# Performance work log

Hardware: AMD Instinct MI355X
Metric: run time of the kernel (lower is better)

Reference implementation:

```python
import jax, jax.numpy as jnp
import numpy as np

DILATIONS = (1, 3, 5)
NUM_HEADS = 2


def _conv(x, w, b, dil=1, pad=0):
    # x: [B,C,H,W], w: [O,I,kh,kw] (OIHW), 'same'-style padding = dilation for k=3
    y = jax.lax.conv_general_dilated(
        x, w, window_strides=(1, 1), padding=[(pad, pad), (pad, pad)],
        rhs_dilation=(dil, dil), dimension_numbers=('NCHW', 'OIHW', 'NCHW'))
    return y + b[None, :, None, None]


def setup_inputs() -> dict:
    key = jax.random.key(0)
    ks = jax.random.split(key, 4)
    B, Cin, H, W = 4, 256, 64, 64
    Cout = 256
    x = jax.random.normal(ks[0], (B, Cin, H, W), dtype=jnp.float32)
    # kaiming-uniform-like init scale
    q_w = jax.random.uniform(ks[1], (Cout, Cin, 3, 3), dtype=jnp.float32,
                             minval=-1.0, maxval=1.0) * np.sqrt(6.0 / (Cin * 9))
    k_w = jax.random.uniform(ks[2], (Cout, Cin, 1, 1), dtype=jnp.float32,
                             minval=-1.0, maxval=1.0) * np.sqrt(6.0 / Cin)
    v_w = jax.random.uniform(ks[3], (Cout, Cin, 1, 1), dtype=jnp.float32,
                             minval=-1.0, maxval=1.0) * np.sqrt(6.0 / Cin)
    q_b = jnp.zeros((Cout,), jnp.float32)
    k_b = jnp.zeros((Cout,), jnp.float32)
    v_b = jnp.zeros((Cout,), jnp.float32)
    return {"x": x, "q_w": q_w, "q_b": q_b, "k_w": k_w, "k_b": k_b,
            "v_w": v_w, "v_b": v_b}


def reference(x, q_w, q_b, k_w, k_b, v_w, v_b):
    B, C, H, W = x.shape
    Cout = q_w.shape[0]
    hd = Cout // NUM_HEADS  # head_dim
    # ds_conv2d: sum of SiLU(dilated conv) over dilations 1,3,5 (padding=dilation)
    q = sum(jax.nn.silu(_conv(x, q_w, q_b, dil=d, pad=d)) for d in DILATIONS)
    k = _conv(x, k_w, k_b)
    v = _conv(x, v_w, v_b)
    N = H * W
    # [B, heads, head_dim, N]
    q = q.reshape(B, NUM_HEADS, hd, N)
    k = k.reshape(B, NUM_HEADS, hd, N)
    v = v.reshape(B, NUM_HEADS, hd, N)
    # energy[b,h,n,m] = sum_d q[b,h,d,n] * k[b,h,d,m]
    energy = jnp.einsum('bhdn,bhdm->bhnm', q, k)
    attn = jax.nn.softmax(energy / jnp.sqrt(jnp.float32(hd)), axis=-1)
    # out[b,h,n,d] = sum_m attn[b,h,n,m] * v[b,h,d,m]; then back to [B,C,H,W]
    out = jnp.einsum('bhnm,bhdm->bhdn', attn, v)
    return out.reshape(B, Cout, H, W)
```

## Files before the change

### kernel.cpp

```cpp
#include <hip/hip_runtime.h>
#include <cstdint>

typedef __attribute__((ext_vector_type(8))) _Float16 f16x8;
typedef __attribute__((ext_vector_type(4))) float f32x4;

#define DEV static __device__ __forceinline__

DEV void gld_lds16(void* lds_base, const void* gsrc) {
  __builtin_amdgcn_global_load_lds(
      (const __attribute__((address_space(1))) unsigned int*)gsrc,
      (__attribute__((address_space(3))) unsigned int*)lds_base,
      16, 0, 0);
}
DEV unsigned short f2h(float f) {
  _Float16 h = (_Float16)f;
  return __builtin_bit_cast(unsigned short, h);
}
DEV unsigned pk2h(float a, float b) {
  auto h2 = __builtin_amdgcn_cvt_pkrtz(a, b);
  return __builtin_bit_cast(unsigned, h2);
}
DEV float v_exp2(float x) { float r; asm("v_exp_f32 %0, %1" : "=v"(r) : "v"(x)); return r; }
DEV float v_rcp(float x) { float r; asm("v_rcp_f32 %0, %1" : "=v"(r) : "v"(x)); return r; }


__global__ __launch_bounds__(256) void k_prep_x(
    const float* __restrict__ x, char* __restrict__ xpad,
    const float* __restrict__ qw, const float* __restrict__ kw, const float* __restrict__ vw,
    unsigned short* __restrict__ Wq, unsigned short* __restrict__ Wk, unsigned short* __restrict__ Wv) {
  __shared__ float xs[32 * 257];
  int h = blockIdx.x, b = blockIdx.y, t = threadIdx.x;
  int gid = (b * 64 + h) * 256 + t;
  const float* q9 = qw + (size_t)gid * 9;
#pragma unroll
  for (int tp = 0; tp < 9; tp++) Wq[tp * 65536 + gid] = f2h(q9[tp]);
  Wk[gid] = f2h(kw[gid]);
  Wv[gid] = f2h(vw[gid]);
  uint4 z = {0, 0, 0, 0};
  char* rowbase = xpad + ((size_t)(b * 74 + h + 5) * 74) * 512;
  for (int i = t; i < 320; i += 256) {
    int col = i >> 5, off = (i & 31) * 16;
    int w = (col < 5) ? col : 64 + col;
    *(uint4*)(rowbase + (size_t)w * 512 + off) = z;
  }
  if (h < 10) {
    int r = (h < 5) ? h : 64 + h;
    char* rb = xpad + ((size_t)(b * 74 + r) * 74) * 512;
    for (int i = t; i < 2368; i += 256) *(uint4*)(rb + (size_t)i * 16) = z;
  }
  const float* xb = x + (size_t)b * 1048576 + h * 64;
  for (int half = 0; half < 2; half++) {
    int w0 = half * 32;
    for (int kk = 0; kk < 32; kk++) {
      int flat = kk * 256 + t;
      int ci = flat >> 5, w = flat & 31;
      xs[w * 257 + ci] = xb[ci * 4096 + w0 + w];
    }
    __syncthreads();
    for (int g = 0; g < 4; g++) {
      int w = g * 8 + (t >> 5);
      int cg = t & 31;
      float v0 = xs[w * 257 + cg * 8 + 0], v1 = xs[w * 257 + cg * 8 + 1];
      float v2 = xs[w * 257 + cg * 8 + 2], v3 = xs[w * 257 + cg * 8 + 3];
      float v4 = xs[w * 257 + cg * 8 + 4], v5 = xs[w * 257 + cg * 8 + 5];
      float v6 = xs[w * 257 + cg * 8 + 6], v7 = xs[w * 257 + cg * 8 + 7];
      uint4 pk;
      pk.x = pk2h(v0, v1);
      pk.y = pk2h(v2, v3);
      pk.z = pk2h(v4, v5);
      pk.w = pk2h(v6, v7);
      *(uint4*)(xpad + ((size_t)((b * 74 + h + 5) * 74) + w0 + w + 5) * 512 + cg * 16) = pk;
    }
    __syncthreads();
  }
}

__global__ __launch_bounds__(256, 2) void k_conv_kv(
    const char* __restrict__ xpad, const unsigned short* __restrict__ Wk,
    const unsigned short* __restrict__ Wv, const float* __restrict__ kb,
    const float* __restrict__ vb, unsigned short* __restrict__ K, unsigned short* __restrict__ V) {
  __shared__ char sm[65536];
  int t = threadIdx.x, lane = t & 63, wid = t >> 6, q4 = lane >> 4, l15 = lane & 15;
  int px0 = blockIdx.x * 128;
  int b = px0 >> 12, nn = px0 & 4095;
  int h = blockIdx.y;
  int mode = blockIdx.z;
  int co0 = h * 128;
  const char* Wsrc = (const char*)(mode ? Wv : Wk);
  int wm = wid & 1, wn = wid >> 1;

#define STAGE_KV(base_, c_)                                                       \
  {                                                                               \
    for (int ch = wid * 1024; ch < 16384; ch += 4096) {                           \
      int o = ch + lane * 16;                                                     \
      int r = o >> 7;                                                             \
      int n = nn + r, hh = n >> 6, ww2 = n & 63;                                  \
      int col = (o & 127) ^ ((r & 7) << 4);                                       \
      gld_lds16((base_) + ch,                                                     \
                xpad + ((size_t)((b * 74 + hh + 5) * 74) + ww2 + 5) * 512 + (c_)*128 + col); \
    }                                                                             \
    for (int ch = wid * 1024; ch < 16384; ch += 4096) {                           \
      int o = ch + lane * 16;                                                     \
      int r = o >> 7;                                                             \
      int col = (o & 127) ^ ((r & 7) << 4);                                       \
      gld_lds16((base_) + 16384 + ch, Wsrc + (co0 + r) * 512 + (c_)*128 + col);   \
    }                                                                             \
  }

  STAGE_KV(sm, 0);
  asm volatile("s_waitcnt vmcnt(0)" ::: "memory");
  __syncthreads();

  f32x4 acc[4][4] = {};
  for (int c = 0; c < 4; c++) {
    char* cb = sm + (c & 1) * 32768;
    if (c < 3) STAGE_KV(sm + ((c & 1) ^ 1) * 32768, c + 1);
    const char* Xs = cb;
    const char* Ws = cb + 16384;
    int xg = mode ? wn : wm;
    int wg = mode ? wm : wn;
#pragma unroll
    for (int kt = 0; kt < 2; kt++) {
      f16x8 xf[4], wf[4];
#pragma unroll
      for (int i = 0; i < 4; i++) {
        int rx = xg * 64 + i * 16 + l15;
        xf[i] = *(const f16x8*)(Xs + ((rx * 128 + kt * 64 + q4 * 16) ^ ((rx & 7) << 4)));
        int rw = wg * 64 + i * 16 + l15;
        wf[i] = *(const f16x8*)(Ws + ((rw * 128 + kt * 64 + q4 * 16) ^ ((rw & 7) << 4)));
      }
#pragma unroll
      for (int m = 0; m < 4; m++)
#pragma unroll
        for (int n = 0; n < 4; n++)
          acc[m][n] = mode ? __builtin_amdgcn_mfma_f32_16x16x32_f16(wf[m], xf[n], acc[m][n], 0, 0, 0)
                           : __builtin_amdgcn_mfma_f32_16x16x32_f16(xf[m], wf[n], acc[m][n], 0, 0, 0);
    }
    asm volatile("s_waitcnt vmcnt(0)" ::: "memory");
    __syncthreads();
  }
#undef STAGE_KV
  int bh = b * 2 + h;
  if (mode == 0) {
#pragma unroll
    for (int m = 0; m < 4; m++)
#pragma unroll
      for (int n = 0; n < 4; n++) {
        int dd = wn * 64 + n * 16 + l15;
        float bias = kb[co0 + dd];
#pragma unroll
        for (int j = 0; j < 4; j++) {
          int npix = nn + wm * 64 + m * 16 + q4 * 4 + j;
          K[(size_t)(bh * 4096 + npix) * 128 + dd] = f2h(acc[m][n][j] + bias);
        }
      }
  } else {
#pragma unroll
    for (int m = 0; m < 4; m++)
#pragma unroll
      for (int j = 0; j < 4; j++) {
        int cr = wm * 64 + m * 16 + q4 * 4 + j;
        float bias = vb[co0 + cr];
#pragma unroll
        for (int n = 0; n < 4; n++) {
          int pc = nn + wn * 64 + (n >> 1) * 32 + (l15 >> 2) * 8 + (n & 1) * 4 + (l15 & 3);
          V[(size_t)(bh * 128 + cr) * 4096 + pc] = f2h(acc[m][n][j] + bias);
        }
      }
  }
}

__global__ __launch_bounds__(512, 2) void k_conv_q(
    const char* __restrict__ xpad, const unsigned short* __restrict__ Wq,
    const float* __restrict__ qb, unsigned short* __restrict__ Q) {
  extern __shared__ char sm[];
  int t = threadIdx.x, lane = t & 63, wid = t >> 6, q4 = lane >> 4, l15 = lane & 15;
  int fblk = blockIdx.x;
  int g = (fblk & 7) * 32 + (fblk >> 3);
  int h2 = g & 31, b = (g >> 5) & 3, ch2 = g >> 7;
  int h0 = h2 * 2;
  int co0 = ch2 * 128;
  int wn = wid & 1, wq = wid >> 1;
  int hr = wq >> 1, wloc = wq & 1;
  const int dil[3] = {1, 3, 5};
  const char* WqB = (const char*)Wq;
  f32x4 accd[3][2][4] = {};

#define STAGE_B(dstbuf, kh_, c_, kw_)                                             \
  {                                                                               \
    const char* src_ = WqB + (size_t)((kh_)*3 + (kw_)) * 131072 + co0 * 512 + (c_)*128; \
    char* dst_ = (dstbuf);                                                        \
    for (int ch = wid * 1024; ch < 16384; ch += 8192) {                           \
      int o = ch + lane * 16;                                                     \
      int r = o >> 7;                                                             \
      int col = (o & 127) ^ ((r & 7) << 4);                                       \
      gld_lds16(dst_ + ch, src_ + r * 512 + col);                                 \
    }                                                                             \
  }

#define STAGE_A_ROW(abase_, slot_, pr_, c_)                                       \
  {                                                                               \
    const char* src_ = xpad + ((size_t)(b * 74 + (pr_)) * 74) * 512 + (c_)*128;   \
    char* dst_ = (abase_) + (slot_)*9472;                                         \
    for (int ch = wid * 1024; ch < 9472; ch += 8192) {                            \
      int o = ch + lane * 16;                                                     \
      if (o < 9472) {                                                             \
        int r = o >> 7;                                                           \
        int col = (o & 127) ^ ((r & 7) << 4);                                     \
        gld_lds16(dst_ + ch, src_ + r * 512 + col);                               \
      }                                                                           \
    }                                                                             \
  }

#define STAGE_A(abase_, kh_, c_)                                                  \
  {                                                                               \
    if ((kh_) == 1) {                                                             \
      for (int s = 0; s < 2; s++) STAGE_A_ROW(abase_, s, h0 + s + 5, c_);         \
    } else {                                                                      \
      for (int di = 0; di < 3; di++)                                              \
        for (int s = 0; s < 2; s++)                                               \
          STAGE_A_ROW(abase_, di * 2 + s, h0 + s + ((kh_)-1) * dil[di] + 5, c_);  \
    }                                                                             \
  }

  STAGE_A(sm + 32768, 0, 0);
  STAGE_B(sm, 0, 0, 0);
  asm volatile("s_waitcnt vmcnt(0)" ::: "memory");
  __syncthreads();

  int curB = 0, curA = 0;
  for (int kh = 0; kh < 3; kh++) {
    for (int c = 0; c < 4; c++) {
      int cn2 = c + 1, khn2 = kh;
      if (cn2 == 4) { cn2 = 0; khn2 = kh + 1; }
      for (int kw = 0; kw < 3; kw++) {
        int kwn = kw + 1, cn = c, khn = kh;
        if (kwn == 3) { kwn = 0; cn = c + 1; if (cn == 4) { cn = 0; khn = kh + 1; } }
        char* Bnext = curB ? sm : sm + 16384;
        if (khn < 3) STAGE_B(Bnext, khn, cn, kwn);
        if (kw == 0 && khn2 < 3) STAGE_A(sm + 32768 + (curA ^ 1) * 56832, khn2, cn2);
        const char* Bc = curB ? sm + 16384 : sm;
        const char* Abase = sm + 32768 + curA * 56832;
        f16x8 bf[4][2];
#pragma unroll
        for (int n = 0; n < 4; n++)
#pragma unroll
          for (int kt = 0; kt < 2; kt++) {
            int rc = wn * 64 + n * 16 + l15;
            bf[n][kt] = *(const f16x8*)(Bc + ((rc * 128 + kt * 64 + q4 * 16) ^ ((rc & 7) << 4)));
          }
#pragma unroll
        for (int di = 0; di < 3; di++) {
          int dw = (kw - 1) * dil[di] + 5;
          const char* Ad = Abase + (kh == 1 ? hr : di * 2 + hr) * 9472;
          f16x8 af[2][2];
#pragma unroll
          for (int m = 0; m < 2; m++)
#pragma unroll
            for (int kt = 0; kt < 2; kt++) {
              int wp = wloc * 32 + m * 16 + l15 + dw;
              af[m][kt] = *(const f16x8*)(Ad + ((wp * 128 + kt * 64 + q4 * 16) ^ ((wp & 7) << 4)));
            }
          __builtin_amdgcn_s_setprio(1);
#pragma unroll
          for (int m = 0; m < 2; m++)
#pragma unroll
            for (int n = 0; n < 4; n++)
#pragma unroll
              for (int kt = 0; kt < 2; kt++)
                accd[di][m][n] = __builtin_amdgcn_mfma_f32_16x16x32_f16(af[m][kt], bf[n][kt], accd[di][m][n], 0, 0, 0);
          __builtin_amdgcn_s_setprio(0);
        }
        asm volatile("s_waitcnt vmcnt(0)" ::: "memory");
        __syncthreads();
        curB ^= 1;
      }
      if (khn2 < 3) curA ^= 1;
    }
  }
#undef STAGE_A
#undef STAGE_A_ROW
#undef STAGE_B
  const float LOG2E = 1.4426950408889634f;
  const float QSCALE = 0.12751879523176862f;
#pragma unroll
  for (int n = 0; n < 4; n++) {
    float bias = qb[co0 + wn * 64 + n * 16 + l15];
#pragma unroll
    for (int m = 0; m < 2; m++)
#pragma unroll
      for (int j = 0; j < 4; j++) {
        float s = 0.f;
#pragma unroll
        for (int di = 0; di < 3; di++) {
          float v = accd[di][m][n][j] + bias;
          s += v * v_rcp(1.0f + v_exp2(-v * LOG2E));
        }
        int w = wloc * 32 + m * 16 + q4 * 4 + j;
        int npix = (h0 + hr) * 64 + w;
        int dd = wn * 64 + n * 16 + l15;
        Q[((size_t)(b * 2 + ch2) * 4096 + npix) * 128 + dd] = f2h(s * QSCALE);
      }
  }
}

__global__ __launch_bounds__(512) void k_attn(
    const unsigned short* __restrict__ Q, const unsigned short* __restrict__ K,
    const unsigned short* __restrict__ V, float* __restrict__ out) {
  extern __shared__ char sm[];
  int t = threadIdx.x, lane = t & 63, wid = t >> 6, q4 = lane >> 4, l15 = lane & 15;
  int half = wid >> 2, wv = wid & 3;
  int fblk = blockIdx.x;
  int g = (fblk & 7) * 32 + (fblk >> 3);
  int nb = g & 31, bh = g >> 5;
  int b = bh >> 1, hh = bh & 1;
  int n0 = nb * 128;
  char* smg = sm + half * 65536;
  const char* Qg = (const char*)(Q + ((size_t)bh * 4096 + n0) * 128);
  const char* Kg = (const char*)(K + (size_t)bh * 4096 * 128) + half * 524288;
  const char* Vg = (const char*)(V + (size_t)bh * 128 * 4096) + half * 4096;
  f16x8 qf[2][4];
#pragma unroll
  for (int nt = 0; nt < 2; nt++)
#pragma unroll
    for (int kt = 0; kt < 4; kt++) {
      int rn = wv * 32 + nt * 16 + l15;
      qf[nt][kt] = *(const f16x8*)(Qg + (size_t)rn * 256 + kt * 64 + q4 * 16);
    }
  const char* pT0 = smg + (((l15 * 256 + 0 * 64 + q4 * 16) ^ (l15 << 4)));
  const char* pT1 = smg + (((l15 * 256 + 1 * 64 + q4 * 16) ^ (l15 << 4)));
  const char* pT2 = smg + (((l15 * 256 + 2 * 64 + q4 * 16) ^ (l15 << 4)));
  const char* pT3 = smg + (((l15 * 256 + 3 * 64 + q4 * 16) ^ (l15 << 4)));
  const char* pU0 = smg + 32768 + (((l15 * 128 + 0 * 64 + q4 * 16) ^ ((l15 & 7) << 4)));
  const char* pU1 = smg + 32768 + (((l15 * 128 + 1 * 64 + q4 * 16) ^ ((l15 & 7) << 4)));
  int ks[4], vs[4], lch[4];
#pragma unroll
  for (int c2 = 0; c2 < 4; c2++) {
    int ch = wv * 1024 + c2 * 4096;
    int o = ch + lane * 16;
    lch[c2] = ch;
    ks[c2] = o ^ (((o >> 8) & 15) << 4);
    int dd = o >> 7;
    vs[c2] = dd * 8192 + ((o & 127) ^ ((dd & 7) << 4));
  }
#pragma unroll
  for (int c2 = 0; c2 < 4; c2++) gld_lds16(smg + lch[c2], Kg + ks[c2]);
#pragma unroll
  for (int c2 = 0; c2 < 4; c2++) gld_lds16(smg + 32768 + lch[c2], Vg + vs[c2]);
  asm volatile("s_waitcnt vmcnt(0)" ::: "memory");
  __syncthreads();
  f32x4 Ofr[8][2] = {};
  float mrun[2] = {-3e38f, -3e38f};
  float lrun[2] = {0.f, 0.f};
  const char* kgp = Kg;
  const char* vgp = Vg;

#define ATTN_ITER(KB, VB, KBN, VBN, do_pf)                                          \
  {                                                                                 \
    if (do_pf) {                                                                    \
      kgp += 16384;                                                                 \
      vgp += 128;                                                                   \
      _Pragma("unroll") for (int c2 = 0; c2 < 4; c2++)                              \
          gld_lds16(smg + (KBN) + lch[c2], kgp + ks[c2]);                           \
      _Pragma("unroll") for (int c2 = 0; c2 < 4; c2++)                              \
          gld_lds16(smg + (VBN) + lch[c2], vgp + vs[c2]);                           \
    }                                                                               \
    f32x4 sT[4][2] = {};                                                            \
    _Pragma("unroll") for (int kt = 0; kt < 4; kt++) {                              \
      const char* pT = (kt == 0) ? pT0 : (kt == 1) ? pT1 : (kt == 2) ? pT2 : pT3;   \
      f16x8 kf[4];                                                                  \
      _Pragma("unroll") for (int mt = 0; mt < 4; mt++)                              \
          kf[mt] = *(const f16x8*)(pT + (KB) + mt * 4096);                          \
      __builtin_amdgcn_s_setprio(1);                                                \
      _Pragma("unroll") for (int mt = 0; mt < 4; mt++)                              \
          _Pragma("unroll") for (int nt = 0; nt < 2; nt++)                          \
              sT[mt][nt] = __builtin_amdgcn_mfma_f32_16x16x32_f16(                  \
                  kf[mt], qf[nt][kt], sT[mt][nt], 0, 0, 0);                         \
      __builtin_amdgcn_s_setprio(0);                                                \
    }                                                                               \
    unsigned U[2][4][2];                                                            \
    _Pragma("unroll") for (int nt = 0; nt < 2; nt++) {                              \
      float mx = sT[0][nt][0];                                                      \
      _Pragma("unroll") for (int mt = 0; mt < 4; mt++)                              \
          _Pragma("unroll") for (int j = 0; j < 4; j++) mx = fmaxf(mx, sT[mt][nt][j]); \
      mx = fmaxf(mx, __shfl_xor(mx, 16));                                           \
      mx = fmaxf(mx, __shfl_xor(mx, 32));                                           \
      float mn = mrun[nt];                                                          \
      if (!__all(mx - mn <= 8.f)) {                                                 \
        mn = fmaxf(mrun[nt], mx);                                                   \
        float al = v_exp2(mrun[nt] - mn);                                           \
        mrun[nt] = mn;                                                              \
        lrun[nt] *= al;                                                             \
        _Pragma("unroll") for (int dt = 0; dt < 8; dt++) Ofr[dt][nt] *= al;         \
      }                                                                             \
      float rs = 0.f;                                                               \
      _Pragma("unroll") for (int mt = 0; mt < 4; mt++) {                            \
        float p0 = v_exp2(sT[mt][nt][0] - mn);                                      \
        float p1 = v_exp2(sT[mt][nt][1] - mn);                                      \
        float p2 = v_exp2(sT[mt][nt][2] - mn);                                      \
        float p3 = v_exp2(sT[mt][nt][3] - mn);                                      \
        rs += (p0 + p1) + (p2 + p3);                                                \
        U[nt][mt][0] = pk2h(p0, p1);                                                \
        U[nt][mt][1] = pk2h(p2, p3);                                                \
      }                                                                             \
      rs += __shfl_xor(rs, 16);                                                     \
      rs += __shfl_xor(rs, 32);                                                     \
      lrun[nt] += rs;                                                               \
    }                                                                               \
    _Pragma("unroll") for (int kt = 0; kt < 2; kt++) {                              \
      const char* pU = kt ? pU1 : pU0;                                              \
      f16x8 pf[2];                                                                  \
      _Pragma("unroll") for (int nt = 0; nt < 2; nt++) {                            \
        uint4 fr;                                                                   \
        fr.x = U[nt][2 * kt][0];                                                    \
        fr.y = U[nt][2 * kt][1];                                                    \
        fr.z = U[nt][2 * kt + 1][0];                                                \
        fr.w = U[nt][2 * kt + 1][1];                                                \
        pf[nt] = __builtin_bit_cast(f16x8, fr);                                     \
      }                                                                             \
      f16x8 vf[8];                                                                  \
      _Pragma("unroll") for (int dt = 0; dt < 8; dt++)                              \
          vf[dt] = *(const f16x8*)(pU + ((VB)-32768) + dt * 2048);                  \
      __builtin_amdgcn_s_setprio(1);                                                \
      _Pragma("unroll") for (int dt = 0; dt < 8; dt++)                              \
          _Pragma("unroll") for (int nt = 0; nt < 2; nt++)                          \
              Ofr[dt][nt] = __builtin_amdgcn_mfma_f32_16x16x32_f16(                 \
                  vf[dt], pf[nt], Ofr[dt][nt], 0, 0, 0);                            \
      __builtin_amdgcn_s_setprio(0);                                                \
    }                                                                               \
    __syncthreads();                                                                \
  }

  for (int it2 = 0; it2 < 16; it2++) {
    ATTN_ITER(0, 32768, 16384, 49152, true);
    ATTN_ITER(16384, 49152, 0, 32768, (it2 < 15));
  }
#undef ATTN_ITER

  float* xch = (float*)sm;
  float* mlx = (float*)(sm + 65536);
  int slot = t & 255;
  if (half == 1) {
#pragma unroll
    for (int dt = 0; dt < 8; dt++)
#pragma unroll
      for (int nt = 0; nt < 2; nt++)
#pragma unroll
        for (int j = 0; j < 4; j++)
          xch[(dt * 8 + nt * 4 + j) * 256 + slot] = Ofr[dt][nt][j];
    mlx[slot] = mrun[0];
    mlx[256 + slot] = mrun[1];
    mlx[512 + slot] = lrun[0];
    mlx[768 + slot] = lrun[1];
  }
  __syncthreads();
  if (half == 0) {
    float m1[2] = {mlx[slot], mlx[256 + slot]};
    float l1[2] = {mlx[512 + slot], mlx[768 + slot]};
    float a0[2], a1[2], li[2];
#pragma unroll
    for (int nt = 0; nt < 2; nt++) {
      float ms = fmaxf(mrun[nt], m1[nt]);
      a0[nt] = v_exp2(mrun[nt] - ms);
      a1[nt] = v_exp2(m1[nt] - ms);
      li[nt] = v_rcp(lrun[nt] * a0[nt] + l1[nt] * a1[nt]);
    }
    float* og = out + (size_t)(b * 256 + hh * 128) * 4096 + n0 + wv * 32;
#pragma unroll
    for (int dt = 0; dt < 8; dt++)
#pragma unroll
      for (int nt = 0; nt < 2; nt++)
#pragma unroll
        for (int j = 0; j < 4; j++) {
          int dd = dt * 16 + q4 * 4 + j;
          float o1v = xch[(dt * 8 + nt * 4 + j) * 256 + slot];
          og[(size_t)dd * 4096 + nt * 16 + l15] =
              (Ofr[dt][nt][j] * a0[nt] + o1v * a1[nt]) * li[nt];
        }
  }
}

extern "C" void kernel_launch(void* const* d_in, const int* in_sizes, int n_in,
                              void* d_out, int out_size, void* d_ws, size_t ws_size,
                              hipStream_t stream) {
  (void)in_sizes; (void)n_in; (void)out_size;
  const float* x  = (const float*)d_in[0];
  const float* qw = (const float*)d_in[1];
  const float* qb = (const float*)d_in[2];
  const float* kw = (const float*)d_in[3];
  const float* kb = (const float*)d_in[4];
  const float* vw = (const float*)d_in[5];
  const float* vb = (const float*)d_in[6];
  char* ws = (char*)d_ws;
  if (ws_size < 37822464) return;
  char* xpad = ws;
  unsigned short* Wq = (unsigned short*)(ws + 11214848);
  unsigned short* Wk = (unsigned short*)(ws + 12394496);
  unsigned short* Wv = (unsigned short*)(ws + 12525568);
  unsigned short* Qb = (unsigned short*)(ws + 12656640);
  unsigned short* Kb = (unsigned short*)(ws + 21045248);
  unsigned short* Vb = (unsigned short*)(ws + 29433856);
  k_prep_x<<<dim3(64, 4), dim3(256), 0, stream>>>(x, xpad, qw, kw, vw, Wq, Wk, Wv);
  k_conv_kv<<<dim3(128, 2, 2), dim3(256), 0, stream>>>(xpad, Wk, Wv, kb, vb, Kb, Vb);
  k_conv_q<<<dim3(256), dim3(512), 146432, stream>>>(xpad, Wq, qb, Qb);
  k_attn<<<dim3(256), dim3(512), 131072, stream>>>(Qb, Kb, Vb, (float*)d_out);
}
```

Before: 155.4 us.

## Software-pipeline QK^T one tile ahead of softmax and PV in attention loop

Restructures the flash-attention inner loop so the QK^T scores for the next key tile are computed while the softmax and PV for the previous tile run, using two score register sets (sTa/sTb). K and V prefetches into LDS are staggered separately so K loads run one stage ahead of V. This is meant to let the score MFMAs overlap the exp and reduction ALU work and shorten dependency stalls. It costs extra VGPRs for the second score buffer, which may reduce occupancy or cause spills.

```diff
diff --git a/kernel.cpp b/kernel.cpp
--- a/kernel.cpp
+++ b/kernel.cpp
@@ -343,46 +343,74 @@
     int dd = o >> 7;
     vs[c2] = dd * 8192 + ((o & 127) ^ ((dd & 7) << 4));
   }
+  f32x4 Ofr[8][2] = {};
+  f32x4 sTa[4][2], sTb[4][2];
+  float mrun[2] = {-3e38f, -3e38f};
+  float lrun[2] = {0.f, 0.f};
+  const f32x4 zf4 = {0.f, 0.f, 0.f, 0.f};
+
 #pragma unroll
   for (int c2 = 0; c2 < 4; c2++) gld_lds16(smg + lch[c2], Kg + ks[c2]);
 #pragma unroll
   for (int c2 = 0; c2 < 4; c2++) gld_lds16(smg + 32768 + lch[c2], Vg + vs[c2]);
   asm volatile("s_waitcnt vmcnt(0)" ::: "memory");
   __syncthreads();
-  f32x4 Ofr[8][2] = {};
-  float mrun[2] = {-3e38f, -3e38f};
-  float lrun[2] = {0.f, 0.f};
-  const char* kgp = Kg;
+  const char* kgp = Kg + 16384;
   const char* vgp = Vg;
-
-#define ATTN_ITER(KB, VB, KBN, VBN, do_pf)                                          \
+#pragma unroll
+  for (int c2 = 0; c2 < 4; c2++) gld_lds16(smg + 16384 + lch[c2], kgp + ks[c2]);
+#pragma unroll
+  for (int mt = 0; mt < 4; mt++)
+#pragma unroll
+    for (int nt = 0; nt < 2; nt++) sTa[mt][nt] = zf4;
+#pragma unroll
+  for (int kt = 0; kt < 4; kt++) {
+    const char* pT = (kt == 0) ? pT0 : (kt == 1) ? pT1 : (kt == 2) ? pT2 : pT3;
+    f16x8 kf[4];
+#pragma unroll
+    for (int mt = 0; mt < 4; mt++) kf[mt] = *(const f16x8*)(pT + mt * 4096);
+#pragma unroll
+    for (int mt = 0; mt < 4; mt++)
+#pragma unroll
+      for (int nt = 0; nt < 2; nt++)
+        sTa[mt][nt] = __builtin_amdgcn_mfma_f32_16x16x32_f16(kf[mt], qf[nt][kt], sTa[mt][nt], 0, 0, 0);
+  }
+  __syncthreads();
+
+#define ATTN_BODY(KSTG, VSTG, KQK, VPV, STPREV, STNEXT, doK, doV, doQK)             \
   {                                                                                 \
-    if (do_pf) {                                                                    \
+    if (doK) {                                                                      \
       kgp += 16384;                                                                 \
+      _Pragma("unroll") for (int c2 = 0; c2 < 4; c2++)                              \
+          gld_lds16(smg + (KSTG) + lch[c2], kgp + ks[c2]);                          \
+    }                                                                               \
+    if (doV) {                                                                      \
       vgp += 128;                                                                   \
       _Pragma("unroll") for (int c2 = 0; c2 < 4; c2++)                              \
-          gld_lds16(smg + (KBN) + lch[c2], kgp + ks[c2]);                           \
-      _Pragma("unroll") for (int c2 = 0; c2 < 4; c2++)                              \
-          gld_lds16(smg + (VBN) + lch[c2], vgp + vs[c2]);                           \
+          gld_lds16(smg + (VSTG) + lch[c2], vgp + vs[c2]);                          \
     }                                                                               \
-    f32x4 sT[4][2] = {};                                                            \
-    _Pragma("unroll") for (int kt = 0; kt < 4; kt++) {                              \
-      const char* pT = (kt == 0) ? pT0 : (kt == 1) ? pT1 : (kt == 2) ? pT2 : pT3;   \
-      f16x8 kf[4];                                                                  \
+    if (doQK) {                                                                     \
       _Pragma("unroll") for (int mt = 0; mt < 4; mt++)                              \
-          kf[mt] = *(const f16x8*)(pT + (KB) + mt * 4096);                          \
-      __builtin_amdgcn_s_setprio(1);                                                \
-      _Pragma("unroll") for (int mt = 0; mt < 4; mt++)                              \
-          _Pragma("unroll") for (int nt = 0; nt < 2; nt++)                          \
-              sT[mt][nt] = __builtin_amdgcn_mfma_f32_16x16x32_f16(                  \
-                  kf[mt], qf[nt][kt], sT[mt][nt], 0, 0, 0);                         \
-      __builtin_amdgcn_s_setprio(0);                                                \
+          _Pragma("unroll") for (int nt = 0; nt < 2; nt++) STNEXT[mt][nt] = zf4;    \
+      _Pragma("unroll") for (int kt = 0; kt < 4; kt++) {                            \
+        const char* pT = (kt == 0) ? pT0 : (kt == 1) ? pT1 : (kt == 2) ? pT2 : pT3; \
+        f16x8 kf[4];                                                                \
+        _Pragma("unroll") for (int mt = 0; mt < 4; mt++)                            \
+            kf[mt] = *(const f16x8*)(pT + (KQK) + mt * 4096);                       \
+        __builtin_amdgcn_s_setprio(1);                                              \
+        _Pragma("unroll") for (int mt = 0; mt < 4; mt++)                            \
+            _Pragma("unroll") for (int nt = 0; nt < 2; nt++)                        \
+                STNEXT[mt][nt] = __builtin_amdgcn_mfma_f32_16x16x32_f16(            \
+                    kf[mt], qf[nt][kt], STNEXT[mt][nt], 0, 0, 0);                   \
+        __builtin_amdgcn_s_setprio(0);                                              \
+      }                                                                             \
     }                                                                               \
     unsigned U[2][4][2];                                                            \
     _Pragma("unroll") for (int nt = 0; nt < 2; nt++) {                              \
-      float mx = sT[0][nt][0];                                                      \
+      float mx = STPREV[0][nt][0];                                                  \
       _Pragma("unroll") for (int mt = 0; mt < 4; mt++)                              \
-          _Pragma("unroll") for (int j = 0; j < 4; j++) mx = fmaxf(mx, sT[mt][nt][j]); \
+          _Pragma("unroll") for (int j = 0; j < 4; j++)                             \
+              mx = fmaxf(mx, STPREV[mt][nt][j]);                                    \
       mx = fmaxf(mx, __shfl_xor(mx, 16));                                           \
       mx = fmaxf(mx, __shfl_xor(mx, 32));                                           \
       float mn = mrun[nt];                                                          \
@@ -395,10 +423,10 @@
       }                                                                             \
       float rs = 0.f;                                                               \
       _Pragma("unroll") for (int mt = 0; mt < 4; mt++) {                            \
-        float p0 = v_exp2(sT[mt][nt][0] - mn);                                      \
-        float p1 = v_exp2(sT[mt][nt][1] - mn);                                      \
-        float p2 = v_exp2(sT[mt][nt][2] - mn);                                      \
-        float p3 = v_exp2(sT[mt][nt][3] - mn);                                      \
+        float p0 = v_exp2(STPREV[mt][nt][0] - mn);                                  \
+        float p1 = v_exp2(STPREV[mt][nt][1] - mn);                                  \
+        float p2 = v_exp2(STPREV[mt][nt][2] - mn);                                  \
+        float p3 = v_exp2(STPREV[mt][nt][3] - mn);                                  \
         rs += (p0 + p1) + (p2 + p3);                                                \
         U[nt][mt][0] = pk2h(p0, p1);                                                \
         U[nt][mt][1] = pk2h(p2, p3);                                                \
@@ -420,7 +448,7 @@
       }                                                                             \
       f16x8 vf[8];                                                                  \
       _Pragma("unroll") for (int dt = 0; dt < 8; dt++)                              \
-          vf[dt] = *(const f16x8*)(pU + ((VB)-32768) + dt * 2048);                  \
+          vf[dt] = *(const f16x8*)(pU + ((VPV)-32768) + dt * 2048);                 \
       __builtin_amdgcn_s_setprio(1);                                                \
       _Pragma("unroll") for (int dt = 0; dt < 8; dt++)                              \
           _Pragma("unroll") for (int nt = 0; nt < 2; nt++)                          \
@@ -432,10 +460,10 @@
   }
 
   for (int it2 = 0; it2 < 16; it2++) {
-    ATTN_ITER(0, 32768, 16384, 49152, true);
-    ATTN_ITER(16384, 49152, 0, 32768, (it2 < 15));
-  }
-#undef ATTN_ITER
+    ATTN_BODY(0, 49152, 16384, 32768, sTa, sTb, (it2 < 15), true, true);
+    ATTN_BODY(16384, 32768, 0, 49152, sTb, sTa, (it2 < 15), (it2 < 15), (it2 < 15));
+  }
+#undef ATTN_BODY
 
   float* xch = (float*)sm;
   float* mlx = (float*)(sm + 65536);
```

New measurement: 154.6 us, median of 2. Within noise of the previous version (-0.5%).
